# Performance work log

Measured on AMD Instinct MI355X. Metric: run time of the kernel, lower is better.

## Reference

```python
import jax, jax.numpy as jnp
import numpy as np

B, T, C, H = 2, 2048, 1024, 16
HD = C // H  # head_dim = 64


def setup_inputs() -> dict:
    key = jax.random.key(0)
    ks = jax.random.split(key, 5)
    x = jax.random.normal(ks[0], (B, T, C), dtype=jnp.float32)
    # realistic rotary tables: cos/sin of position*inv_freq, shape (T, HD//2)
    inv_freq = 1.0 / (10000.0 ** (jnp.arange(0, HD, 2, dtype=jnp.float32) / HD))
    ang = jnp.arange(T, dtype=jnp.float32)[:, None] * inv_freq[None, :]
    cos, sin = jnp.cos(ang), jnp.sin(ang)
    w_attn = jax.random.normal(ks[1], (C, 3 * C), dtype=jnp.float32) * (C ** -0.5)
    b_attn = jnp.zeros((3 * C,), dtype=jnp.float32)
    w_proj = jax.random.normal(ks[2], (C, C), dtype=jnp.float32) * (C ** -0.5)
    b_proj = jnp.zeros((C,), dtype=jnp.float32)
    return {"x": x, "cos": cos, "sin": sin, "w_attn": w_attn, "b_attn": b_attn,
            "w_proj": w_proj, "b_proj": b_proj}


def _apply_rotary(x, cos, sin):
    # x: (B, H, T, HD); cos/sin: (T, HD//2) broadcast over B,H
    x_even = x[..., ::2]
    x_odd = x[..., 1::2]
    rot = jnp.stack((x_even * cos - x_odd * sin, x_even * sin + x_odd * cos), axis=-1)
    return rot.reshape(*x.shape[:-1], x.shape[-1])


def reference(x, cos, sin, w_attn, b_attn, w_proj, b_proj):
    b, t, c = x.shape
    qkv = x @ w_attn + b_attn                       # (B, T, 3C)
    q, k, v = jnp.split(qkv, 3, axis=-1)
    # (B, T, C) -> (B, H, T, HD)
    def to_heads(z):
        return z.reshape(b, t, H, HD).transpose(0, 2, 1, 3)
    q, k, v = to_heads(q), to_heads(k), to_heads(v)
    q = _apply_rotary(q, cos, sin)
    k = _apply_rotary(k, cos, sin)
    scale = 1.0 / jnp.sqrt(jnp.asarray(HD, dtype=x.dtype))
    scores = jnp.einsum('bhqd,bhkd->bhqk', q, k) * scale
    causal = jnp.tril(jnp.ones((t, t), dtype=bool))
    scores = jnp.where(causal, scores, jnp.asarray(-jnp.inf, dtype=scores.dtype))
    attn = jax.nn.softmax(scores, axis=-1)
    y = jnp.einsum('bhqk,bhkd->bhqd', attn, v)      # (B, H, T, HD)
    y = y.transpose(0, 2, 1, 3).reshape(b, t, c)
    return y @ w_proj + b_proj
```

## Files before the change

### kernel.cpp

```cpp
#include <hip/hip_runtime.h>
#include <hip/hip_bf16.h>
#include <math.h>

#define Bsz 2
#define Tseq 2048
#define Cdim 1024
#define Hn 16
#define HDim 64
#define Mrows 4096
#define N3 3072
#define QSCALE 0.1803368801111137f

typedef __bf16 bf16_t;
typedef __bf16 bf16x4 __attribute__((ext_vector_type(4)));
typedef __bf16 bf16x8 __attribute__((ext_vector_type(8)));
typedef float floatx4 __attribute__((ext_vector_type(4)));

__device__ __forceinline__ void async16(const void* g, void* l) {
    __builtin_amdgcn_global_load_lds(
        (const __attribute__((address_space(1))) void*)g,
        (__attribute__((address_space(3))) void*)l, 16, 0, 0);
}

__global__ __launch_bounds__(256) void prep_kernel(
    const float* __restrict__ x, const float* __restrict__ w_attn,
    const float* __restrict__ w_proj, bf16_t* __restrict__ xb,
    bf16_t* __restrict__ waT, bf16_t* __restrict__ wpT)
{
    __shared__ float Ts[32][33];
    const int bid = blockIdx.x;
    if (bid < 2048) {
        size_t g = (size_t)bid * 256 + threadIdx.x;
        float4 a = *(const float4*)(x + g * 8);
        float4 b = *(const float4*)(x + g * 8 + 4);
        bf16x8 o;
        o[0] = (bf16_t)a.x; o[1] = (bf16_t)a.y; o[2] = (bf16_t)a.z; o[3] = (bf16_t)a.w;
        o[4] = (bf16_t)b.x; o[5] = (bf16_t)b.y; o[6] = (bf16_t)b.z; o[7] = (bf16_t)b.w;
        *(bf16x8*)(xb + g * 8) = o;
        return;
    }
    const float* in; bf16_t* out; int R, C, bx, by;
    if (bid < 5120) {
        int t = bid - 2048; in = w_attn; out = waT; R = Cdim; C = N3;
        bx = t % 96; by = t / 96;
    } else {
        int t = bid - 5120; in = w_proj; out = wpT; R = Cdim; C = Cdim;
        bx = t & 31; by = t >> 5;
    }
    int c0 = bx << 5, r0 = by << 5;
    int lr = threadIdx.x >> 3, lc = (threadIdx.x & 7) << 2;
    float4 v = *(const float4*)(in + (size_t)(r0 + lr) * C + c0 + lc);
    Ts[lr][lc] = v.x; Ts[lr][lc + 1] = v.y; Ts[lr][lc + 2] = v.z; Ts[lr][lc + 3] = v.w;
    __syncthreads();
    bf16x4 o;
    o[0] = (bf16_t)Ts[lc + 0][lr]; o[1] = (bf16_t)Ts[lc + 1][lr];
    o[2] = (bf16_t)Ts[lc + 2][lr]; o[3] = (bf16_t)Ts[lc + 3][lr];
    *(bf16x4*)(out + (size_t)(c0 + lr) * R + r0 + lc) = o;
}

#define QSTAGE(AD, BD, KO) do {                                              \
    _Pragma("unroll") for (int _it = 0; _it < 2; ++_it) {                    \
        int _ci = (w << 7) + (_it << 6) + lane;                              \
        int _row = _ci >> 2, _cq = (_ci & 3) ^ (_row & 3);                   \
        async16(Ag + (size_t)_row * Cdim + (KO) + _cq * 8,                   \
                (AD) + ((w << 7) + (_it << 6)) * 8);                         \
        async16(Bg + (size_t)_row * Cdim + (KO) + _cq * 8,                   \
                (BD) + ((w << 7) + (_it << 6)) * 8);                         \
    } } while (0)

#define QCOMP(AC, BC) do {                                                   \
    bf16x8 _af[4], _bf[4];                                                   \
    _Pragma("unroll") for (int _i = 0; _i < 4; _i++) {                       \
        int _row = (wy << 6) + (_i << 4) + lm;                               \
        int _cq = quad ^ (lm & 3);                                           \
        _af[_i] = *(const bf16x8*)&(AC)[_row * 32 + _cq * 8];                \
        int _rb = (wx << 6) + (_i << 4) + lm;                                \
        _bf[_i] = *(const bf16x8*)&(BC)[_rb * 32 + _cq * 8];                 \
    }                                                                        \
    _Pragma("unroll") for (int _i = 0; _i < 4; _i++)                         \
        _Pragma("unroll") for (int _j = 0; _j < 4; _j++)                     \
            acc[_i][_j] = __builtin_amdgcn_mfma_f32_16x16x32_bf16(           \
                _af[_i], _bf[_j], acc[_i][_j], 0, 0, 0);                     \
    } while (0)

#define QWAIT4 do { asm volatile("s_waitcnt vmcnt(4)" ::: "memory");         \
    __builtin_amdgcn_s_barrier(); __builtin_amdgcn_sched_barrier(0); } while (0)
#define QWAIT0 do { asm volatile("s_waitcnt vmcnt(0)" ::: "memory");         \
    __builtin_amdgcn_s_barrier(); __builtin_amdgcn_sched_barrier(0); } while (0)

__global__ __launch_bounds__(256) void gemm_qkv(
    const bf16_t* __restrict__ xb, const bf16_t* __restrict__ waT,
    const float* __restrict__ bias, const float* __restrict__ cosb,
    const float* __restrict__ sinb,
    bf16_t* __restrict__ qb, bf16_t* __restrict__ kb, bf16_t* __restrict__ vt)
{
    __shared__ bf16_t As0[4096], As1[4096], As2[4096];
    __shared__ bf16_t Bs0[4096], Bs1[4096], Bs2[4096];
    const int tid = threadIdx.x;
    const int lane = tid & 63, w = tid >> 6;
    const int lm = lane & 15, quad = lane >> 4;
    const int wy = w >> 1, wx = w & 1;
    const int bid = blockIdx.x;
    const int xcd = bid & 7, i5 = bid >> 3;
    const int gn = ((xcd & 1) * 12) + (i5 % 12);
    const int gm = ((xcd >> 1) * 8) + (i5 / 12);
    const int m0 = gm << 7, n0 = gn << 7;

    const floatx4 fz = {0.f, 0.f, 0.f, 0.f};
    floatx4 acc[4][4];
    #pragma unroll
    for (int i = 0; i < 4; i++)
        #pragma unroll
        for (int j = 0; j < 4; j++) acc[i][j] = fz;

    const bf16_t* Ag = xb + (size_t)m0 * Cdim;
    const bf16_t* Bg = waT + (size_t)n0 * Cdim;

    QSTAGE(As0, Bs0, 0);
    QSTAGE(As1, Bs1, 32);

    for (int m = 0; m < 10; ++m) {
        const int t = 3 * m;
        QWAIT4; QSTAGE(As2, Bs2, (t + 2) << 5); QCOMP(As0, Bs0);
        QWAIT4; QSTAGE(As0, Bs0, (t + 3) << 5); QCOMP(As1, Bs1);
        QWAIT4; QSTAGE(As1, Bs1, (t + 4) << 5); QCOMP(As2, Bs2);
    }
    QWAIT4; QCOMP(As0, Bs0);
    QWAIT0; QCOMP(As1, Bs1);

    const int sec = n0 >> 10;
    const int mb = m0 + (wy << 6);
    const int nb = n0 + (wx << 6);
    #pragma unroll
    for (int i = 0; i < 4; i++) {
        int mrow0 = mb + (i << 4) + (quad << 2);
        int b = mrow0 >> 11, t0 = mrow0 & 2047;
        #pragma unroll
        for (int j = 0; j < 4; j++) {
            int n = nb + (j << 4) + lm;
            float bi = bias[n];
            int rel = n & 1023;
            int h = rel >> 6, hd = rel & 63;
            if (sec == 2) {
                int tp = (t0 & ~31) | (((t0 >> 2) & 3) << 3) | (((t0 >> 4) & 1) << 2);
                bf16x4 pk;
                #pragma unroll
                for (int r = 0; r < 4; r++) pk[r] = (bf16_t)(acc[i][j][r] + bi);
                *(bf16x4*)&vt[((size_t)(b * Hn + h) * HDim + hd) * Tseq + tp] = pk;
            } else {
                bf16_t* dst = (sec == 0) ? qb : kb;
                const int ih = hd >> 1;
                const bool ev = !(hd & 1);
                #pragma unroll
                for (int r = 0; r < 4; r++) {
                    int t = t0 + r;
                    float v = acc[i][j][r] + bi;
                    float x = __shfl_xor(v, 1);
                    float c = cosb[t * 32 + ih], s = sinb[t * 32 + ih];
                    float rv = ev ? (v * c - x * s) : (x * s + v * c);
                    if (sec == 0) rv *= QSCALE;
                    dst[((size_t)(b * Hn + h) * Tseq + t) * HDim + hd] = (bf16_t)rv;
                }
            }
        }
    }
}

__global__ __launch_bounds__(256) void attn_mfma(
    const bf16_t* __restrict__ qb, const bf16_t* __restrict__ kb,
    const bf16_t* __restrict__ vt, bf16_t* __restrict__ yb)
{
    __shared__ bf16_t Ks[3][64 * 64];
    __shared__ bf16_t VTs[3][64 * 64];

    const int bid = blockIdx.x;
    const int jt = 31 - (bid >> 5);
    const int bh = bid & 31;
    const int b = bh >> 4, h = bh & 15;
    const int tid = threadIdx.x;
    const int w4 = tid >> 6, lane = tid & 63, lm = lane & 15, quad = lane >> 4;
    const int nk = jt + 1;

    const bf16_t* Kg0 = kb + (size_t)bh * Tseq * HDim;
    const bf16_t* Vg0 = vt + (size_t)bh * HDim * Tseq;

    const int qq = (jt << 6) + (w4 << 4) + lm;
    bf16x8 qf[2];
    {
        const bf16_t* Qg = qb + ((size_t)bh * Tseq + qq) * HDim;
        #pragma unroll
        for (int ks = 0; ks < 2; ++ks)
            qf[ks] = *(const bf16x8*)(Qg + (ks << 5) + (quad << 3));
    }
    asm volatile("s_waitcnt vmcnt(0)" ::: "memory");

    auto stagef = [&](int tile, int buf) {
        const bf16_t* Kg = Kg0 + (size_t)(tile << 6) * HDim;
        const bf16_t* Vg = Vg0 + (tile << 6);
        #pragma unroll
        for (int it = 0; it < 2; ++it) {
            int ci = (it << 8) + tid;
            int row = ci >> 3, cq = (ci & 7) ^ (row & 7);
            async16(Kg + row * HDim + cq * 8, &Ks[buf][((it << 8) + (w4 << 6)) * 8]);
            async16(Vg + (size_t)row * Tseq + cq * 8, &VTs[buf][((it << 8) + (w4 << 6)) * 8]);
        }
    };

    stagef(0, 0);
    if (nk > 1) stagef(1, 1);

    const floatx4 fz = {0.f, 0.f, 0.f, 0.f};
    floatx4 o_[4];
    #pragma unroll
    for (int f = 0; f < 4; ++f) o_[f] = fz;
    float l_ = 0.f;

    int cb = 0, sb = 2;
    for (int kt = 0; kt < nk; ++kt) {
        if (kt == nk - 1) { asm volatile("s_waitcnt vmcnt(0)" ::: "memory"); }
        else             { asm volatile("s_waitcnt vmcnt(4)" ::: "memory"); }
        __builtin_amdgcn_s_barrier();
        __builtin_amdgcn_sched_barrier(0);
        if (kt + 2 < nk) stagef(kt + 2, sb);

        floatx4 st[4];
        #pragma unroll
        for (int sub = 0; sub < 4; ++sub) st[sub] = fz;
        #pragma unroll
        for (int ks = 0; ks < 2; ++ks) {
            bf16x8 kf[4];
            #pragma unroll
            for (int sub = 0; sub < 4; ++sub) {
                int krow = (sub << 4) + lm;
                int kc = ((ks << 2) + quad) ^ (krow & 7);
                kf[sub] = *(const bf16x8*)&Ks[cb][krow * 64 + kc * 8];
            }
            #pragma unroll
            for (int sub = 0; sub < 4; ++sub)
                st[sub] = __builtin_amdgcn_mfma_f32_16x16x32_bf16(
                    kf[sub], qf[ks], st[sub], 0, 0, 0);
        }

        const bool dm = (kt == jt);
        bf16x8 pf[2];
        float rs = 0.f;
        #pragma unroll
        for (int cc = 0; cc < 2; ++cc)
            #pragma unroll
            for (int jj = 0; jj < 8; ++jj) {
                int sub = (cc << 1) + (jj >> 2), r = jj & 3;
                float val = st[sub][r];
                if (dm) {
                    int key = (kt << 6) + (sub << 4) + (quad << 2) + r;
                    if (key > qq) val = -3e38f;
                }
                float p = exp2f(val);
                rs += p;
                pf[cc][jj] = (bf16_t)p;
            }
        rs += __shfl_xor(rs, 16);
        rs += __shfl_xor(rs, 32);
        l_ += rs;

        #pragma unroll
        for (int cc = 0; cc < 2; ++cc) {
            bf16x8 vf[4];
            #pragma unroll
            for (int f = 0; f < 4; ++f) {
                int vrow = (f << 4) + lm;
                int vc = ((cc << 2) + quad) ^ (vrow & 7);
                vf[f] = *(const bf16x8*)&VTs[cb][vrow * 64 + vc * 8];
            }
            #pragma unroll
            for (int f = 0; f < 4; ++f)
                o_[f] = __builtin_amdgcn_mfma_f32_16x16x32_bf16(
                    vf[f], pf[cc], o_[f], 0, 0, 0);
        }
        sb = cb; cb = (cb == 2) ? 0 : cb + 1;
    }

    {
        float inv = 1.f / l_;
        size_t base = ((size_t)(b * Tseq) + qq) * Cdim + (h << 6) + (quad << 2);
        #pragma unroll
        for (int f = 0; f < 4; ++f) {
            bf16x4 ov;
            #pragma unroll
            for (int r = 0; r < 4; ++r) ov[r] = (bf16_t)(o_[f][r] * inv);
            *(bf16x4*)&yb[base + (f << 4)] = ov;
        }
    }
}

__global__ __launch_bounds__(256) void gemm_proj(
    const bf16_t* __restrict__ yb, const bf16_t* __restrict__ wpT,
    const float* __restrict__ bias, float* __restrict__ out)
{
    __shared__ bf16_t As[128 * 32];
    __shared__ bf16_t Bs[64 * 32];
    const int tid = threadIdx.x;
    const int lane = tid & 63, w = tid >> 6;
    const int lm = lane & 15, quad = lane >> 4;
    const int wy = w >> 1, wx = w & 1;
    const int bid = blockIdx.x;
    const int xcd = bid & 7, idx = bid >> 3;
    const int gm = (xcd << 2) + (idx >> 4);
    const int gn = idx & 15;
    const int m0 = gm << 7, n0 = gn << 6;

    const floatx4 fz = {0.f, 0.f, 0.f, 0.f};
    floatx4 acc[4][2];
    #pragma unroll
    for (int i = 0; i < 4; i++)
        #pragma unroll
        for (int j = 0; j < 2; j++) acc[i][j] = fz;

    const bf16_t* Ag = yb + (size_t)m0 * Cdim;
    const bf16_t* Bg = wpT + (size_t)n0 * Cdim;

    for (int k0 = 0; k0 < Cdim; k0 += 32) {
        #pragma unroll
        for (int it = 0; it < 2; ++it) {
            int ci = (w << 7) + (it << 6) + lane;
            int row = ci >> 2, cq = (ci & 3) ^ (row & 3);
            async16(Ag + (size_t)row * Cdim + k0 + cq * 8, As + ((w << 7) + (it << 6)) * 8);
        }
        {
            int ci = tid;
            int row = ci >> 2, cq = (ci & 3) ^ (row & 3);
            async16(Bg + (size_t)row * Cdim + k0 + cq * 8, Bs + (w << 6) * 8);
        }
        __syncthreads();
        bf16x8 af[4], bfr[2];
        #pragma unroll
        for (int i = 0; i < 4; i++) {
            int row = (wy << 6) + (i << 4) + lm;
            int cq = quad ^ (lm & 3);
            af[i] = *(const bf16x8*)&As[row * 32 + cq * 8];
        }
        #pragma unroll
        for (int j = 0; j < 2; j++) {
            int row = (wx << 5) + (j << 4) + lm;
            int cq = quad ^ (lm & 3);
            bfr[j] = *(const bf16x8*)&Bs[row * 32 + cq * 8];
        }
        #pragma unroll
        for (int i = 0; i < 4; i++)
            #pragma unroll
            for (int j = 0; j < 2; j++)
                acc[i][j] = __builtin_amdgcn_mfma_f32_16x16x32_bf16(af[i], bfr[j], acc[i][j], 0, 0, 0);
        __syncthreads();
    }

    const int mb = m0 + (wy << 6);
    const int nb = n0 + (wx << 5);
    #pragma unroll
    for (int i = 0; i < 4; i++) {
        int mrow0 = mb + (i << 4) + (quad << 2);
        #pragma unroll
        for (int j = 0; j < 2; j++) {
            int n = nb + (j << 4) + lm;
            float bi = bias[n];
            #pragma unroll
            for (int r = 0; r < 4; r++)
                out[(size_t)(mrow0 + r) * Cdim + n] = acc[i][j][r] + bi;
        }
    }
}

extern "C" void kernel_launch(void* const* d_in, const int* in_sizes, int n_in,
                              void* d_out, int out_size, void* d_ws, size_t ws_size,
                              hipStream_t stream) {
    const float* x      = (const float*)d_in[0];
    const float* cosb   = (const float*)d_in[1];
    const float* sinb   = (const float*)d_in[2];
    const float* w_attn = (const float*)d_in[3];
    const float* b_attn = (const float*)d_in[4];
    const float* w_proj = (const float*)d_in[5];
    const float* b_proj = (const float*)d_in[6];

    char* ws = (char*)d_ws;
    bf16_t* xb  = (bf16_t*)(ws);
    bf16_t* waT = (bf16_t*)(ws + (size_t)(8 << 20));
    bf16_t* wpT = (bf16_t*)(ws + (size_t)(14 << 20));
    bf16_t* qb  = (bf16_t*)(ws + (size_t)(16 << 20));
    bf16_t* kb  = (bf16_t*)(ws + (size_t)(24 << 20));
    bf16_t* vtb = (bf16_t*)(ws + (size_t)(32 << 20));
    bf16_t* yb  = (bf16_t*)(ws + (size_t)(40 << 20));

    prep_kernel<<<6144, 256, 0, stream>>>(x, w_attn, w_proj, xb, waT, wpT);
    gemm_qkv<<<768, 256, 0, stream>>>(xb, waT, b_attn, cosb, sinb, qb, kb, vtb);
    attn_mfma<<<1024, 256, 0, stream>>>(qb, kb, vtb, yb);
    gemm_proj<<<512, 256, 0, stream>>>(yb, wpT, b_proj, (float*)d_out);
}
```

Measured before the change: 192.0 us.

## Move triple-buffered pipeline from QKV GEMM to proj GEMM; MFMA row-sum in attention

Result: faster. 175.1 us (-8.8%).

```diff
diff --git a/kernel.cpp b/kernel.cpp
--- a/kernel.cpp
+++ b/kernel.cpp
@@ -58,44 +58,14 @@
     *(bf16x4*)(out + (size_t)(c0 + lr) * R + r0 + lc) = o;
 }
 
-#define QSTAGE(AD, BD, KO) do {                                              \
-    _Pragma("unroll") for (int _it = 0; _it < 2; ++_it) {                    \
-        int _ci = (w << 7) + (_it << 6) + lane;                              \
-        int _row = _ci >> 2, _cq = (_ci & 3) ^ (_row & 3);                   \
-        async16(Ag + (size_t)_row * Cdim + (KO) + _cq * 8,                   \
-                (AD) + ((w << 7) + (_it << 6)) * 8);                         \
-        async16(Bg + (size_t)_row * Cdim + (KO) + _cq * 8,                   \
-                (BD) + ((w << 7) + (_it << 6)) * 8);                         \
-    } } while (0)
-
-#define QCOMP(AC, BC) do {                                                   \
-    bf16x8 _af[4], _bf[4];                                                   \
-    _Pragma("unroll") for (int _i = 0; _i < 4; _i++) {                       \
-        int _row = (wy << 6) + (_i << 4) + lm;                               \
-        int _cq = quad ^ (lm & 3);                                           \
-        _af[_i] = *(const bf16x8*)&(AC)[_row * 32 + _cq * 8];                \
-        int _rb = (wx << 6) + (_i << 4) + lm;                                \
-        _bf[_i] = *(const bf16x8*)&(BC)[_rb * 32 + _cq * 8];                 \
-    }                                                                        \
-    _Pragma("unroll") for (int _i = 0; _i < 4; _i++)                         \
-        _Pragma("unroll") for (int _j = 0; _j < 4; _j++)                     \
-            acc[_i][_j] = __builtin_amdgcn_mfma_f32_16x16x32_bf16(           \
-                _af[_i], _bf[_j], acc[_i][_j], 0, 0, 0);                     \
-    } while (0)
-
-#define QWAIT4 do { asm volatile("s_waitcnt vmcnt(4)" ::: "memory");         \
-    __builtin_amdgcn_s_barrier(); __builtin_amdgcn_sched_barrier(0); } while (0)
-#define QWAIT0 do { asm volatile("s_waitcnt vmcnt(0)" ::: "memory");         \
-    __builtin_amdgcn_s_barrier(); __builtin_amdgcn_sched_barrier(0); } while (0)
-
 __global__ __launch_bounds__(256) void gemm_qkv(
     const bf16_t* __restrict__ xb, const bf16_t* __restrict__ waT,
     const float* __restrict__ bias, const float* __restrict__ cosb,
     const float* __restrict__ sinb,
     bf16_t* __restrict__ qb, bf16_t* __restrict__ kb, bf16_t* __restrict__ vt)
 {
-    __shared__ bf16_t As0[4096], As1[4096], As2[4096];
-    __shared__ bf16_t Bs0[4096], Bs1[4096], Bs2[4096];
+    __shared__ bf16_t As[128 * 32];
+    __shared__ bf16_t Bs[128 * 32];
     const int tid = threadIdx.x;
     const int lane = tid & 63, w = tid >> 6;
     const int lm = lane & 15, quad = lane >> 4;
@@ -116,17 +86,35 @@
     const bf16_t* Ag = xb + (size_t)m0 * Cdim;
     const bf16_t* Bg = waT + (size_t)n0 * Cdim;
 
-    QSTAGE(As0, Bs0, 0);
-    QSTAGE(As1, Bs1, 32);
-
-    for (int m = 0; m < 10; ++m) {
-        const int t = 3 * m;
-        QWAIT4; QSTAGE(As2, Bs2, (t + 2) << 5); QCOMP(As0, Bs0);
-        QWAIT4; QSTAGE(As0, Bs0, (t + 3) << 5); QCOMP(As1, Bs1);
-        QWAIT4; QSTAGE(As1, Bs1, (t + 4) << 5); QCOMP(As2, Bs2);
-    }
-    QWAIT4; QCOMP(As0, Bs0);
-    QWAIT0; QCOMP(As1, Bs1);
+    for (int k0 = 0; k0 < Cdim; k0 += 32) {
+        #pragma unroll
+        for (int it = 0; it < 2; ++it) {
+            int ci = (w << 7) + (it << 6) + lane;
+            int row = ci >> 2, cq = (ci & 3) ^ (row & 3);
+            async16(Ag + (size_t)row * Cdim + k0 + cq * 8, As + ((w << 7) + (it << 6)) * 8);
+            async16(Bg + (size_t)row * Cdim + k0 + cq * 8, Bs + ((w << 7) + (it << 6)) * 8);
+        }
+        __syncthreads();
+        bf16x8 af[4], bfr[4];
+        #pragma unroll
+        for (int i = 0; i < 4; i++) {
+            int row = (wy << 6) + (i << 4) + lm;
+            int cq = quad ^ (lm & 3);
+            af[i] = *(const bf16x8*)&As[row * 32 + cq * 8];
+        }
+        #pragma unroll
+        for (int j = 0; j < 4; j++) {
+            int row = (wx << 6) + (j << 4) + lm;
+            int cq = quad ^ (lm & 3);
+            bfr[j] = *(const bf16x8*)&Bs[row * 32 + cq * 8];
+        }
+        #pragma unroll
+        for (int i = 0; i < 4; i++)
+            #pragma unroll
+            for (int j = 0; j < 4; j++)
+                acc[i][j] = __builtin_amdgcn_mfma_f32_16x16x32_bf16(af[i], bfr[j], acc[i][j], 0, 0, 0);
+        __syncthreads();
+    }
 
     const int sec = n0 >> 10;
     const int mb = m0 + (wy << 6);
@@ -213,7 +201,9 @@
     floatx4 o_[4];
     #pragma unroll
     for (int f = 0; f < 4; ++f) o_[f] = fz;
-    float l_ = 0.f;
+    floatx4 o_l = fz;
+    const bf16_t one_b = (bf16_t)1.f;
+    const bf16x8 onesf = {one_b, one_b, one_b, one_b, one_b, one_b, one_b, one_b};
 
     int cb = 0, sb = 2;
     for (int kt = 0; kt < nk; ++kt) {
@@ -243,7 +233,6 @@
 
         const bool dm = (kt == jt);
         bf16x8 pf[2];
-        float rs = 0.f;
         #pragma unroll
         for (int cc = 0; cc < 2; ++cc)
             #pragma unroll
@@ -254,13 +243,8 @@
                     int key = (kt << 6) + (sub << 4) + (quad << 2) + r;
                     if (key > qq) val = -3e38f;
                 }
-                float p = exp2f(val);
-                rs += p;
-                pf[cc][jj] = (bf16_t)p;
+                pf[cc][jj] = (bf16_t)exp2f(val);
             }
-        rs += __shfl_xor(rs, 16);
-        rs += __shfl_xor(rs, 32);
-        l_ += rs;
 
         #pragma unroll
         for (int cc = 0; cc < 2; ++cc) {
@@ -275,12 +259,14 @@
             for (int f = 0; f < 4; ++f)
                 o_[f] = __builtin_amdgcn_mfma_f32_16x16x32_bf16(
                     vf[f], pf[cc], o_[f], 0, 0, 0);
+            o_l = __builtin_amdgcn_mfma_f32_16x16x32_bf16(
+                onesf, pf[cc], o_l, 0, 0, 0);
         }
         sb = cb; cb = (cb == 2) ? 0 : cb + 1;
     }
 
     {
-        float inv = 1.f / l_;
+        float inv = 1.f / o_l[0];
         size_t base = ((size_t)(b * Tseq) + qq) * Cdim + (h << 6) + (quad << 2);
         #pragma unroll
         for (int f = 0; f < 4; ++f) {
@@ -291,13 +277,50 @@
         }
     }
 }
+
+#define PSTAGE(AD, BD, KO) do {                                              \
+    _Pragma("unroll") for (int _it = 0; _it < 2; ++_it) {                    \
+        int _ci = (w << 7) + (_it << 6) + lane;                              \
+        int _row = _ci >> 2, _cq = (_ci & 3) ^ (_row & 3);                   \
+        async16(Ag + (size_t)_row * Cdim + (KO) + _cq * 8,                   \
+                (AD) + ((w << 7) + (_it << 6)) * 8);                         \
+    }                                                                        \
+    {                                                                        \
+        int _ci = tid;                                                       \
+        int _row = _ci >> 2, _cq = (_ci & 3) ^ (_row & 3);                   \
+        async16(Bg + (size_t)_row * Cdim + (KO) + _cq * 8,                   \
+                (BD) + (w << 6) * 8);                                        \
+    } } while (0)
+
+#define PCOMP(AC, BC) do {                                                   \
+    bf16x8 _af[4], _bf[2];                                                   \
+    _Pragma("unroll") for (int _i = 0; _i < 4; _i++) {                       \
+        int _row = (wy << 6) + (_i << 4) + lm;                               \
+        int _cq = quad ^ (lm & 3);                                           \
+        _af[_i] = *(const bf16x8*)&(AC)[_row * 32 + _cq * 8];                \
+    }                                                                        \
+    _Pragma("unroll") for (int _j = 0; _j < 2; _j++) {                       \
+        int _row = (wx << 5) + (_j << 4) + lm;                               \
+        int _cq = quad ^ (lm & 3);                                           \
+        _bf[_j] = *(const bf16x8*)&(BC)[_row * 32 + _cq * 8];                \
+    }                                                                        \
+    _Pragma("unroll") for (int _i = 0; _i < 4; _i++)                         \
+        _Pragma("unroll") for (int _j = 0; _j < 2; _j++)                     \
+            acc[_i][_j] = __builtin_amdgcn_mfma_f32_16x16x32_bf16(           \
+                _af[_i], _bf[_j], acc[_i][_j], 0, 0, 0);                     \
+    } while (0)
+
+#define PWAIT3 do { asm volatile("s_waitcnt vmcnt(3)" ::: "memory");         \
+    __builtin_amdgcn_s_barrier(); __builtin_amdgcn_sched_barrier(0); } while (0)
+#define PWAIT0 do { asm volatile("s_waitcnt vmcnt(0)" ::: "memory");         \
+    __builtin_amdgcn_s_barrier(); __builtin_amdgcn_sched_barrier(0); } while (0)
 
 __global__ __launch_bounds__(256) void gemm_proj(
     const bf16_t* __restrict__ yb, const bf16_t* __restrict__ wpT,
     const float* __restrict__ bias, float* __restrict__ out)
 {
-    __shared__ bf16_t As[128 * 32];
-    __shared__ bf16_t Bs[64 * 32];
+    __shared__ bf16_t As0[4096], As1[4096], As2[4096];
+    __shared__ bf16_t Bs0[2048], Bs1[2048], Bs2[2048];
     const int tid = threadIdx.x;
     const int lane = tid & 63, w = tid >> 6;
     const int lm = lane & 15, quad = lane >> 4;
@@ -318,39 +341,17 @@
     const bf16_t* Ag = yb + (size_t)m0 * Cdim;
     const bf16_t* Bg = wpT + (size_t)n0 * Cdim;
 
-    for (int k0 = 0; k0 < Cdim; k0 += 32) {
-        #pragma unroll
-        for (int it = 0; it < 2; ++it) {
-            int ci = (w << 7) + (it << 6) + lane;
-            int row = ci >> 2, cq = (ci & 3) ^ (row & 3);
-            async16(Ag + (size_t)row * Cdim + k0 + cq * 8, As + ((w << 7) + (it << 6)) * 8);
-        }
-        {
-            int ci = tid;
-            int row = ci >> 2, cq = (ci & 3) ^ (row & 3);
-            async16(Bg + (size_t)row * Cdim + k0 + cq * 8, Bs + (w << 6) * 8);
-        }
-        __syncthreads();
-        bf16x8 af[4], bfr[2];
-        #pragma unroll
-        for (int i = 0; i < 4; i++) {
-            int row = (wy << 6) + (i << 4) + lm;
-            int cq = quad ^ (lm & 3);
-            af[i] = *(const bf16x8*)&As[row * 32 + cq * 8];
-        }
-        #pragma unroll
-        for (int j = 0; j < 2; j++) {
-            int row = (wx << 5) + (j << 4) + lm;
-            int cq = quad ^ (lm & 3);
-            bfr[j] = *(const bf16x8*)&Bs[row * 32 + cq * 8];
-        }
-        #pragma unroll
-        for (int i = 0; i < 4; i++)
-            #pragma unroll
-            for (int j = 0; j < 2; j++)
-                acc[i][j] = __builtin_amdgcn_mfma_f32_16x16x32_bf16(af[i], bfr[j], acc[i][j], 0, 0, 0);
-        __syncthreads();
-    }
+    PSTAGE(As0, Bs0, 0);
+    PSTAGE(As1, Bs1, 32);
+
+    for (int m = 0; m < 10; ++m) {
+        const int t = 3 * m;
+        PWAIT3; PSTAGE(As2, Bs2, (t + 2) << 5); PCOMP(As0, Bs0);
+        PWAIT3; PSTAGE(As0, Bs0, (t + 3) << 5); PCOMP(As1, Bs1);
+        PWAIT3; PSTAGE(As1, Bs1, (t + 4) << 5); PCOMP(As2, Bs2);
+    }
+    PWAIT3; PCOMP(As0, Bs0);
+    PWAIT0; PCOMP(As1, Bs1);
 
     const int mb = m0 + (wy << 6);
     const int nb = n0 + (wx << 5);
```
